# Kernel optimization log

Measured on AMD Instinct MI355X. Metric: run time of the kernel, lower is better.

Reference implementation:

```python
import jax, jax.numpy as jnp
import numpy as np

H = 1024      # hidden_dim
F = 4 * H     # expert FFN dim
E = 16        # num_experts
K = 4         # num_experts_per_token


def setup_inputs() -> dict:
    key = jax.random.key(0)
    ks = jax.random.split(key, 10)
    s = 0.02
    return {
        "x": jax.random.normal(ks[0], (2, 1024, H), dtype=jnp.float32),
        # router: Linear(H,H) -> ReLU -> Linear(H,E)
        "Wr1": jax.random.normal(ks[1], (H, H), dtype=jnp.float32) * s,
        "br1": jnp.zeros((H,), dtype=jnp.float32),
        "Wr2": jax.random.normal(ks[2], (H, E), dtype=jnp.float32) * s,
        "br2": jnp.zeros((E,), dtype=jnp.float32),
        # stacked experts: Linear(H,4H) -> GELU -> Linear(4H,H)
        "W1": jax.random.normal(ks[3], (E, H, F), dtype=jnp.float32) * s,
        "b1": jnp.zeros((E, F), dtype=jnp.float32),
        "W2": jax.random.normal(ks[4], (E, F, H), dtype=jnp.float32) * s,
        "b2": jnp.zeros((E, H), dtype=jnp.float32),
    }


def reference(x, Wr1, br1, Wr2, br2, W1, b1, W2, b2):
    B, S, Hd = x.shape
    xf = x.reshape(-1, Hd)                       # [T, H]
    T = xf.shape[0]
    # router logits
    logits = jnp.maximum(xf @ Wr1 + br1, 0.0) @ Wr2 + br2   # [T, E]
    # top-k routing: softmax over the k selected logits
    topw, topi = jax.lax.top_k(logits, K)                    # [T, K]
    topw = jax.nn.softmax(topw, axis=-1)
    # dense combine weights c[t, e] = sum_k topw[t,k] * 1[topi[t,k]==e]
    c = jnp.zeros((T, E), dtype=xf.dtype)
    c = c.at[jnp.arange(T)[:, None], topi].add(topw)         # [T, E]
    # all-experts dense MLP (exact GELU, matching nn.GELU default)
    h = jax.nn.gelu(jnp.einsum('th,ehf->etf', xf, W1) + b1[:, None, :],
                    approximate=False)                       # [E, T, F]
    y = jnp.einsum('etf,efh->eth', h, W2) + b2[:, None, :]   # [E, T, H]
    out = jnp.einsum('eth,te->th', y, c)                     # [T, H]
    return out.reshape(B, S, Hd)
```

## Files before the change

### kernel.cpp

```cpp
#include <hip/hip_runtime.h>
#include <hip/hip_bf16.h>

#define T_TOK 2048
#define H_DIM 1024
#define F_DIM 4096
#define E_NUM 16
#define K_TOP 4

typedef float    floatx4 __attribute__((ext_vector_type(4)));
typedef _Float16 f16x8   __attribute__((ext_vector_type(8)));
typedef __fp16   fp16v2  __attribute__((ext_vector_type(2)));

#define MiB (1024ull * 1024ull)
#define LOGIT_OFF ((size_t)0)
#define OFFS_OFF  (256ull * 1024)
#define TOKS_OFF  (320ull * 1024)
#define WSL_OFF   (384ull * 1024)
#define STK_OFF   (448ull * 1024)
#define TILEE_OFF (512ull * 1024)
#define TILEM_OFF (TILEE_OFF + 512)
#define TILEC_OFF (TILEM_OFF + 512)
#define XH_OFF    (1ull * MiB)
#define HBUF_OFF  (8ull * MiB)
#define YBUF_OFF  (72ull * MiB)
#define WS_NEED_FAST (96ull * MiB)

__device__ __forceinline__ void gload16(const void* g, void* l) {
  __builtin_amdgcn_global_load_lds(
      (const __attribute__((address_space(1))) unsigned int*)g,
      (__attribute__((address_space(3))) unsigned int*)l, 16, 0, 0);
}

__device__ __forceinline__ float gelu_fast(float v) {
  float z = 0.7978845608028654f * (v + 0.044715f * v * v * v);
  float e = __expf(2.f * z);
  float t = 1.f - 2.f / (e + 1.f);
  return 0.5f * v * (1.f + t);
}

__device__ __forceinline__ void cast_x_body(int blk, const float* __restrict__ x,
                                            _Float16* __restrict__ xh) {
  int i = blk * 256 + threadIdx.x;
  const floatx4* xin = reinterpret_cast<const floatx4*>(x) + (size_t)i * 2;
  floatx4 a = xin[0], b = xin[1];
  f16x8 o;
  o[0] = (_Float16)a[0]; o[1] = (_Float16)a[1]; o[2] = (_Float16)a[2]; o[3] = (_Float16)a[3];
  o[4] = (_Float16)b[0]; o[5] = (_Float16)b[1]; o[6] = (_Float16)b[2]; o[7] = (_Float16)b[3];
  *reinterpret_cast<f16x8*>(xh + (size_t)i * 8) = o;
}

__device__ __forceinline__ void router_gemm1_body(
    int m0, int n0, const float* __restrict__ x, const float* __restrict__ Wr1,
    const float* __restrict__ br1, float* __restrict__ hrf, char* smem) {
  _Float16 (*Ah)[40] = (_Float16(*)[40])(smem);
  _Float16 (*Al)[40] = (_Float16(*)[40])(smem + 5120);
  _Float16 (*Bh)[40] = (_Float16(*)[40])(smem + 10240);
  _Float16 (*Bl)[40] = (_Float16(*)[40])(smem + 15360);
  int tid = threadIdx.x;
  int arow = tid >> 2, achk = tid & 3;
  const float* Arow = x + (size_t)(m0 + arow) * H_DIM + achk * 8;
  int brow = tid >> 3, bq = tid & 7;

  floatx4 acc[2][2];
#pragma unroll
  for (int i = 0; i < 2; i++)
#pragma unroll
    for (int j = 0; j < 2; j++) acc[i][j] = (floatx4){0.f, 0.f, 0.f, 0.f};

  int wv = tid >> 6, lane = tid & 63;
  int wm = wv >> 1, wn = wv & 1;
  int lrow = lane & 15, lk = (lane >> 4) * 8;

  for (int k0 = 0; k0 < H_DIM; k0 += 32) {
    floatx4 a0 = *reinterpret_cast<const floatx4*>(Arow + k0);
    floatx4 a1 = *reinterpret_cast<const floatx4*>(Arow + k0 + 4);
    f16x8 hv, lv;
#pragma unroll
    for (int j = 0; j < 4; j++) {
      _Float16 hi = (_Float16)a0[j]; hv[j] = hi; lv[j] = (_Float16)(a0[j] - (float)hi);
      _Float16 hi2 = (_Float16)a1[j]; hv[4 + j] = hi2; lv[4 + j] = (_Float16)(a1[j] - (float)hi2);
    }
    *reinterpret_cast<f16x8*>(&Ah[arow][achk * 8]) = hv;
    *reinterpret_cast<f16x8*>(&Al[arow][achk * 8]) = lv;
    const float* wp = Wr1 + (size_t)(k0 + brow) * H_DIM + n0 + bq * 4;
    floatx4 w0 = *reinterpret_cast<const floatx4*>(wp);
    floatx4 w1 = *reinterpret_cast<const floatx4*>(wp + 32);
#pragma unroll
    for (int i = 0; i < 4; i++) {
      _Float16 h0 = (_Float16)w0[i];
      Bh[bq * 4 + i][brow] = h0; Bl[bq * 4 + i][brow] = (_Float16)(w0[i] - (float)h0);
      _Float16 h1 = (_Float16)w1[i];
      Bh[32 + bq * 4 + i][brow] = h1; Bl[32 + bq * 4 + i][brow] = (_Float16)(w1[i] - (float)h1);
    }
    __syncthreads();

    f16x8 ah0 = *reinterpret_cast<const f16x8*>(&Ah[32 * wm + lrow][lk]);
    f16x8 ah1 = *reinterpret_cast<const f16x8*>(&Ah[32 * wm + 16 + lrow][lk]);
    f16x8 al0 = *reinterpret_cast<const f16x8*>(&Al[32 * wm + lrow][lk]);
    f16x8 al1 = *reinterpret_cast<const f16x8*>(&Al[32 * wm + 16 + lrow][lk]);
    f16x8 bh0 = *reinterpret_cast<const f16x8*>(&Bh[32 * wn + lrow][lk]);
    f16x8 bh1 = *reinterpret_cast<const f16x8*>(&Bh[32 * wn + 16 + lrow][lk]);
    f16x8 bl0 = *reinterpret_cast<const f16x8*>(&Bl[32 * wn + lrow][lk]);
    f16x8 bl1 = *reinterpret_cast<const f16x8*>(&Bl[32 * wn + 16 + lrow][lk]);

    acc[0][0] = __builtin_amdgcn_mfma_f32_16x16x32_f16(ah0, bh0, acc[0][0], 0, 0, 0);
    acc[0][0] = __builtin_amdgcn_mfma_f32_16x16x32_f16(ah0, bl0, acc[0][0], 0, 0, 0);
    acc[0][0] = __builtin_amdgcn_mfma_f32_16x16x32_f16(al0, bh0, acc[0][0], 0, 0, 0);
    acc[0][1] = __builtin_amdgcn_mfma_f32_16x16x32_f16(ah0, bh1, acc[0][1], 0, 0, 0);
    acc[0][1] = __builtin_amdgcn_mfma_f32_16x16x32_f16(ah0, bl1, acc[0][1], 0, 0, 0);
    acc[0][1] = __builtin_amdgcn_mfma_f32_16x16x32_f16(al0, bh1, acc[0][1], 0, 0, 0);
    acc[1][0] = __builtin_amdgcn_mfma_f32_16x16x32_f16(ah1, bh0, acc[1][0], 0, 0, 0);
    acc[1][0] = __builtin_amdgcn_mfma_f32_16x16x32_f16(ah1, bl0, acc[1][0], 0, 0, 0);
    acc[1][0] = __builtin_amdgcn_mfma_f32_16x16x32_f16(al1, bh0, acc[1][0], 0, 0, 0);
    acc[1][1] = __builtin_amdgcn_mfma_f32_16x16x32_f16(ah1, bh1, acc[1][1], 0, 0, 0);
    acc[1][1] = __builtin_amdgcn_mfma_f32_16x16x32_f16(ah1, bl1, acc[1][1], 0, 0, 0);
    acc[1][1] = __builtin_amdgcn_mfma_f32_16x16x32_f16(al1, bh1, acc[1][1], 0, 0, 0);
    __syncthreads();
  }

#pragma unroll
  for (int am = 0; am < 2; am++) {
#pragma unroll
    for (int bn = 0; bn < 2; bn++) {
      int col = n0 + 32 * wn + 16 * bn + lrow;
      float bv = br1[col];
#pragma unroll
      for (int r = 0; r < 4; r++) {
        int rowt = 32 * wm + 16 * am + (lane >> 4) * 4 + r;
        float v = acc[am][bn][r] + bv;
        hrf[(size_t)(m0 + rowt) * H_DIM + col] = fmaxf(v, 0.f);
      }
    }
  }
}

#define P1_RG 512
#define P1_CX 1024
#define P1_TOTAL (P1_RG + P1_CX)
__global__ __launch_bounds__(256) void fusedA_kernel(
    const float* __restrict__ x, const float* __restrict__ Wr1, const float* __restrict__ br1,
    float* __restrict__ hrf, _Float16* __restrict__ xh) {
  __shared__ __align__(16) char smem[20480];
  int bid = blockIdx.x;
  if (bid < P1_RG) {
    router_gemm1_body((bid >> 4) * 64, (bid & 15) * 64, x, Wr1, br1, hrf, smem);
  } else {
    cast_x_body(bid - P1_RG, x, xh);
  }
}

__global__ __launch_bounds__(256) void router_logits_kernel(
    const float* __restrict__ hrf, const float* __restrict__ Wr2,
    const float* __restrict__ br2, float* __restrict__ logits) {
  int t = blockIdx.x * 4 + (threadIdx.x >> 6);
  int lane = threadIdx.x & 63;
  float acc[E_NUM];
#pragma unroll
  for (int e = 0; e < E_NUM; e++) acc[e] = 0.f;
  const float* hr = hrf + (size_t)t * H_DIM;
#pragma unroll 4
  for (int i = 0; i < H_DIM / 64; i++) {
    int k = lane + 64 * i;
    float a = hr[k];
    const floatx4* w4 = reinterpret_cast<const floatx4*>(Wr2 + (size_t)k * E_NUM);
    floatx4 w0 = w4[0], w1 = w4[1], w2 = w4[2], w3 = w4[3];
#pragma unroll
    for (int j = 0; j < 4; j++) {
      acc[j]      += a * w0[j];
      acc[4 + j]  += a * w1[j];
      acc[8 + j]  += a * w2[j];
      acc[12 + j] += a * w3[j];
    }
  }
#pragma unroll
  for (int e = 0; e < E_NUM; e++) {
    float v = acc[e];
    for (int off = 32; off > 0; off >>= 1) v += __shfl_xor(v, off);
    if (lane == e) logits[(size_t)t * E_NUM + e] = v + br2[e];
  }
}

__global__ __launch_bounds__(1024) void routing_kernel(
    const float* __restrict__ logits, int* __restrict__ offs,
    int* __restrict__ toks, float* __restrict__ wsl, int* __restrict__ stk,
    int* __restrict__ tileE, int* __restrict__ tileM, int* __restrict__ tileC) {
  __shared__ int cnt[E_NUM], cur[E_NUM], loff[E_NUM + 1];
  int tid = threadIdx.x;
  if (tid < E_NUM) { cnt[tid] = 0; cur[tid] = 0; }
  __syncthreads();
  int ti[2][K_TOP]; float tw[2][K_TOP];
#pragma unroll
  for (int u = 0; u < 2; u++) {
    int t = u * 1024 + tid;
    float lg[E_NUM];
#pragma unroll
    for (int e = 0; e < E_NUM; e++) lg[e] = logits[(size_t)t * E_NUM + e];
    unsigned int used = 0;
    float vals[K_TOP];
#pragma unroll
    for (int k = 0; k < K_TOP; k++) {
      float best = -1e30f; int bi = 0;
#pragma unroll
      for (int e = 0; e < E_NUM; e++) {
        if (!((used >> e) & 1u) && lg[e] > best) { best = lg[e]; bi = e; }
      }
      used |= (1u << bi);
      vals[k] = best; ti[u][k] = bi;
    }
    float m = vals[0], s = 0.f;
#pragma unroll
    for (int k = 0; k < K_TOP; k++) { tw[u][k] = expf(vals[k] - m); s += tw[u][k]; }
    float inv = 1.f / s;
#pragma unroll
    for (int k = 0; k < K_TOP; k++) {
      tw[u][k] *= inv;
      atomicAdd(&cnt[ti[u][k]], 1);
    }
  }
  __syncthreads();
  if (tid == 0) {
    int acc = 0;
    loff[0] = 0; offs[0] = 0;
    for (int e = 0; e < E_NUM; e++) { acc += cnt[e]; loff[e + 1] = acc; offs[e + 1] = acc; }
    int idx = 0;
    for (int e = 0; e < E_NUM; e++) {
      for (int m0 = 0; m0 < cnt[e]; m0 += 128) { tileE[idx] = e; tileM[idx] = m0; idx++; }
    }
    tileC[0] = idx;
  }
  __syncthreads();
#pragma unroll
  for (int u = 0; u < 2; u++) {
    int t = u * 1024 + tid;
#pragma unroll
    for (int k = 0; k < K_TOP; k++) {
      int e = ti[u][k];
      int pos = atomicAdd(&cur[e], 1);
      int slot = loff[e] + pos;
      toks[slot] = t;
      wsl[slot] = tw[u][k];
      stk[t * K_TOP + k] = slot;
    }
  }
}

__global__ void combine_kernel(const _Float16* __restrict__ ybuf, const int* __restrict__ stk,
                               float* __restrict__ out) {
  int i = blockIdx.x * 256 + threadIdx.x;
  size_t p = (size_t)i * 8;
  int t = (int)(p >> 10);
  int h = (int)(p & 1023);
  float s[8] = {0.f, 0.f, 0.f, 0.f, 0.f, 0.f, 0.f, 0.f};
#pragma unroll
  for (int k = 0; k < K_TOP; k++) {
    int slot = stk[t * K_TOP + k];
    f16x8 v = *reinterpret_cast<const f16x8*>(ybuf + (size_t)slot * H_DIM + h);
#pragma unroll
    for (int j = 0; j < 8; j++) s[j] += (float)v[j];
  }
  floatx4 o0 = {s[0], s[1], s[2], s[3]};
  floatx4 o1 = {s[4], s[5], s[6], s[7]};
  *reinterpret_cast<floatx4*>(out + p) = o0;
  *reinterpret_cast<floatx4*>(out + p + 4) = o1;
}

template <int KK, int ACT, bool GATHER, bool SCALE>
__device__ __forceinline__ void moe_gemm_body(
    int ti, int n0, const _Float16* __restrict__ A, const float* __restrict__ Bf,
    const float* __restrict__ bias, _Float16* __restrict__ Out,
    const int* __restrict__ offsets, const int* __restrict__ toklist,
    const float* __restrict__ wslot, const int* __restrict__ tileE,
    const int* __restrict__ tileM, const int* __restrict__ tileC,
    int N, char* smem) {
  if (ti >= tileC[0]) return;
  const int K = KK;
  int e = tileE[ti], m0 = tileM[ti];
  int base = offsets[e], cnt = offsets[e + 1] - base;

  _Float16 (*As)[128][32] = reinterpret_cast<_Float16(*)[128][32]>(smem);
  float (*Bs)[32][128] = reinterpret_cast<float(*)[32][128]>(smem + 24576);

  int tid = threadIdx.x;
  int w = tid >> 6, lane = tid & 63;
  int wm = w >> 1, wn = w & 1;
  int lrow = lane & 15, hi = lane >> 4;

  int ar0 = w * 32 + (lane >> 2);
  int ar1 = ar0 + 16;
  int ach = (((lane & 3) ^ ((lane >> 3) & 3))) * 8;
  int mr0 = m0 + ar0; if (mr0 >= cnt) mr0 = cnt - 1;
  int mr1 = m0 + ar1; if (mr1 >= cnt) mr1 = cnt - 1;
  const _Float16* gA0 = A + (long)(GATHER ? toklist[base + mr0] : (base + mr0)) * K + ach;
  const _Float16* gA1 = A + (long)(GATHER ? toklist[base + mr1] : (base + mr1)) * K + ach;
  const float* Bfe = Bf + (size_t)e * (size_t)K * (size_t)N;
  const float* gB = Bfe + (size_t)(8 * w + (lane >> 5)) * N + n0 +
                    ((((lane & 31) ^ ((w & 1) << 2))) << 2);

  int phys8 = ((lane >> 4) ^ ((lrow >> 1) & 3)) * 8;
  int bswz = (hi & 1) << 4;

#define STAGE3(buf, kk) do { \
    gload16(gA0 + (kk), &As[buf][w * 32][0]); \
    gload16(gA1 + (kk), &As[buf][w * 32 + 16][0]); \
    gload16(gB + (size_t)(kk) * N,         &Bs[buf][8 * w + 0][0]); \
    gload16(gB + (size_t)(kk) * N + 2 * N, &Bs[buf][8 * w + 2][0]); \
    gload16(gB + (size_t)(kk) * N + 4 * N, &Bs[buf][8 * w + 4][0]); \
    gload16(gB + (size_t)(kk) * N + 6 * N, &Bs[buf][8 * w + 6][0]); \
  } while (0)

#define COMPUTE3(buf) do { \
    f16x8 a[4], b[4]; \
    _Pragma("unroll") \
    for (int i = 0; i < 4; i++) \
      a[i] = *reinterpret_cast<const f16x8*>(&As[buf][wm * 64 + i * 16 + lrow][phys8]); \
    _Pragma("unroll") \
    for (int i = 0; i < 4; i++) { \
      int pcol = (wn * 64 + i * 16 + lrow) ^ bswz; \
      float f0 = Bs[buf][hi * 8 + 0][pcol]; \
      float f1 = Bs[buf][hi * 8 + 1][pcol]; \
      float f2 = Bs[buf][hi * 8 + 2][pcol]; \
      float f3 = Bs[buf][hi * 8 + 3][pcol]; \
      float f4 = Bs[buf][hi * 8 + 4][pcol]; \
      float f5 = Bs[buf][hi * 8 + 5][pcol]; \
      float f6 = Bs[buf][hi * 8 + 6][pcol]; \
      float f7 = Bs[buf][hi * 8 + 7][pcol]; \
      union { fp16v2 h[4]; f16x8 v; } u; \
      u.h[0] = __builtin_amdgcn_cvt_pkrtz(f0, f1); \
      u.h[1] = __builtin_amdgcn_cvt_pkrtz(f2, f3); \
      u.h[2] = __builtin_amdgcn_cvt_pkrtz(f4, f5); \
      u.h[3] = __builtin_amdgcn_cvt_pkrtz(f6, f7); \
      b[i] = u.v; \
    } \
    __builtin_amdgcn_s_setprio(1); \
    _Pragma("unroll") \
    for (int i = 0; i < 4; i++) \
      _Pragma("unroll") \
      for (int j = 0; j < 4; j++) \
        acc[i][j] = __builtin_amdgcn_mfma_f32_16x16x32_f16(a[i], b[j], acc[i][j], 0, 0, 0); \
    __builtin_amdgcn_s_setprio(0); \
  } while (0)

  floatx4 acc[4][4];
#pragma unroll
  for (int i = 0; i < 4; i++)
#pragma unroll
    for (int j = 0; j < 4; j++) acc[i][j] = (floatx4){0.f, 0.f, 0.f, 0.f};

  constexpr int nk = KK / 32;
  STAGE3(0, 0);
  STAGE3(1, 32);

#pragma unroll 3
  for (int it = 0; it < nk - 1; ++it) {
    asm volatile("s_waitcnt vmcnt(6)" ::: "memory");
    __builtin_amdgcn_s_barrier();
    if (it + 2 < nk) STAGE3((it + 2) % 3, (it + 2) * 32);
    COMPUTE3(it % 3);
  }
  asm volatile("s_waitcnt vmcnt(0)" ::: "memory");
  __builtin_amdgcn_s_barrier();
  COMPUTE3((nk - 1) % 3);

#undef STAGE3
#undef COMPUTE3

  const float* be = bias + (size_t)e * N;
#pragma unroll
  for (int fm = 0; fm < 4; fm++) {
#pragma unroll
    for (int fn = 0; fn < 4; fn++) {
      int col = n0 + wn * 64 + fn * 16 + lrow;
      float bv = be[col];
#pragma unroll
      for (int r = 0; r < 4; r++) {
        int rowt = wm * 64 + fm * 16 + (lane >> 4) * 4 + r;
        int mg = m0 + rowt;
        if (mg < cnt) {
          float v = acc[fm][fn][r] + bv;
          if (ACT == 2) v = gelu_fast(v);
          long orow = base + mg;
          if (SCALE) v *= wslot[orow];
          Out[orow * (long)N + col] = (_Float16)v;
        }
      }
    }
  }
}

__global__ __launch_bounds__(256) void moe_gemm1_kernel(
    const _Float16* __restrict__ xh, const float* __restrict__ W1,
    const float* __restrict__ b1, _Float16* __restrict__ hbuf,
    const int* __restrict__ offsets, const int* __restrict__ toklist,
    const int* __restrict__ tileE, const int* __restrict__ tileM, const int* __restrict__ tileC) {
  __shared__ __align__(16) char smem[73728];
  int x = blockIdx.x;
  int ti = (x & 7) * 10 + (x >> 3);
  moe_gemm_body<H_DIM, 2, true, false>(ti, blockIdx.y * 128, xh, W1, b1, hbuf,
                                       offsets, toklist, nullptr, tileE, tileM, tileC,
                                       F_DIM, smem);
}

__global__ __launch_bounds__(256) void moe_gemm2_kernel(
    const _Float16* __restrict__ hbuf, const float* __restrict__ W2,
    const float* __restrict__ b2, _Float16* __restrict__ ybuf,
    const int* __restrict__ offsets, const float* __restrict__ wslot,
    const int* __restrict__ tileE, const int* __restrict__ tileM, const int* __restrict__ tileC) {
  __shared__ __align__(16) char smem[73728];
  int x = blockIdx.x;
  int ti = (x & 7) * 10 + (x >> 3);
  moe_gemm_body<F_DIM, 0, false, true>(ti, blockIdx.y * 128, hbuf, W2, b2, ybuf,
                                       offsets, nullptr, wslot, tileE, tileM, tileC,
                                       H_DIM, smem);
}

template <int ACT, bool GATHER, bool OFFS, bool SCALE>
__global__ __launch_bounds__(256) void moe_gemm(
    const _Float16* __restrict__ A, const float* __restrict__ W,
    const float* __restrict__ bias, _Float16* __restrict__ Out,
    const int* __restrict__ offsets, const int* __restrict__ toklist,
    const float* __restrict__ wslot, int M, int N, int K) {
  int e = blockIdx.z;
  int base = 0, cnt = M;
  if (OFFS) { base = offsets[e]; cnt = offsets[e + 1] - base; }
  int m0 = blockIdx.y * 64;
  if (m0 >= cnt) return;
  int n0 = blockIdx.x * 64;
  const float* We = W + (size_t)e * K * N;
  const float* be = bias + (size_t)e * N;

  __shared__ _Float16 As[64][40];
  __shared__ _Float16 Bs[64][40];

  int tid = threadIdx.x;
  int arow = tid >> 2, achk = tid & 3;
  int am_idx = m0 + arow; if (am_idx > cnt - 1) am_idx = cnt - 1;
  long arowg = GATHER ? (long)toklist[base + am_idx] : (long)(base + am_idx);
  const _Float16* Arow = A + arowg * (long)K + achk * 8;

  int brow = tid >> 3, bq = tid & 7;

  floatx4 acc[2][2];
#pragma unroll
  for (int i = 0; i < 2; i++)
#pragma unroll
    for (int j = 0; j < 2; j++) acc[i][j] = (floatx4){0.f, 0.f, 0.f, 0.f};

  int wv = tid >> 6, lane = tid & 63;
  int wm = wv >> 1, wn = wv & 1;
  int lrow = lane & 15, lk = (lane >> 4) * 8;

  for (int k0 = 0; k0 < K; k0 += 32) {
    *reinterpret_cast<f16x8*>(&As[arow][achk * 8]) = *reinterpret_cast<const f16x8*>(Arow + k0);
    const float* wp = We + (size_t)(k0 + brow) * N + n0 + bq * 4;
    floatx4 w0 = *reinterpret_cast<const floatx4*>(wp);
    floatx4 w1 = *reinterpret_cast<const floatx4*>(wp + 32);
#pragma unroll
    for (int i = 0; i < 4; i++) {
      Bs[bq * 4 + i][brow]      = (_Float16)w0[i];
      Bs[32 + bq * 4 + i][brow] = (_Float16)w1[i];
    }
    __syncthreads();

    f16x8 a0 = *reinterpret_cast<const f16x8*>(&As[32 * wm + lrow][lk]);
    f16x8 a1 = *reinterpret_cast<const f16x8*>(&As[32 * wm + 16 + lrow][lk]);
    f16x8 b0 = *reinterpret_cast<const f16x8*>(&Bs[32 * wn + lrow][lk]);
    f16x8 b1 = *reinterpret_cast<const f16x8*>(&Bs[32 * wn + 16 + lrow][lk]);
    acc[0][0] = __builtin_amdgcn_mfma_f32_16x16x32_f16(a0, b0, acc[0][0], 0, 0, 0);
    acc[0][1] = __builtin_amdgcn_mfma_f32_16x16x32_f16(a0, b1, acc[0][1], 0, 0, 0);
    acc[1][0] = __builtin_amdgcn_mfma_f32_16x16x32_f16(a1, b0, acc[1][0], 0, 0, 0);
    acc[1][1] = __builtin_amdgcn_mfma_f32_16x16x32_f16(a1, b1, acc[1][1], 0, 0, 0);
    __syncthreads();
  }

#pragma unroll
  for (int am = 0; am < 2; am++) {
#pragma unroll
    for (int bn = 0; bn < 2; bn++) {
      int col = n0 + 32 * wn + 16 * bn + lrow;
      float bv = be[col];
#pragma unroll
      for (int r = 0; r < 4; r++) {
        int rowt = 32 * wm + 16 * am + (lane >> 4) * 4 + r;
        int mg = m0 + rowt;
        if (mg < cnt) {
          float v = acc[am][bn][r] + bv;
          if (ACT == 2) v = gelu_fast(v);
          long orow = base + mg;
          if (SCALE) v *= wslot[orow];
          Out[orow * (long)N + col] = (_Float16)v;
        }
      }
    }
  }
}

__global__ void cast_x_kernel(const float* __restrict__ x, _Float16* __restrict__ xh) {
  cast_x_body(blockIdx.x, x, xh);
}

__global__ __launch_bounds__(256) void router_gemm1_kernel(
    const float* __restrict__ x, const float* __restrict__ Wr1,
    const float* __restrict__ br1, float* __restrict__ hrf) {
  __shared__ __align__(16) char smem[20480];
  router_gemm1_body(blockIdx.y * 64, blockIdx.x * 64, x, Wr1, br1, hrf, smem);
}

extern "C" void kernel_launch(void* const* d_in, const int* in_sizes, int n_in,
                              void* d_out, int out_size, void* d_ws, size_t ws_size,
                              hipStream_t stream) {
  const float* x   = (const float*)d_in[0];
  const float* Wr1 = (const float*)d_in[1];
  const float* br1 = (const float*)d_in[2];
  const float* Wr2 = (const float*)d_in[3];
  const float* br2 = (const float*)d_in[4];
  const float* W1  = (const float*)d_in[5];
  const float* b1  = (const float*)d_in[6];
  const float* W2  = (const float*)d_in[7];
  const float* b2  = (const float*)d_in[8];
  float* out = (float*)d_out;

  char* ws = (char*)d_ws;
  float* logits = (float*)(ws + LOGIT_OFF);
  int*   offs   = (int*)(ws + OFFS_OFF);
  int*   toks   = (int*)(ws + TOKS_OFF);
  float* wsl    = (float*)(ws + WSL_OFF);
  int*   stk    = (int*)(ws + STK_OFF);
  int*   tileE  = (int*)(ws + TILEE_OFF);
  int*   tileM  = (int*)(ws + TILEM_OFF);
  int*   tileC  = (int*)(ws + TILEC_OFF);
  _Float16* xh   = (_Float16*)(ws + XH_OFF);
  float*    hrf  = (float*)(ws + HBUF_OFF);
  _Float16* hbuf = (_Float16*)(ws + HBUF_OFF);
  _Float16* ybuf = (_Float16*)(ws + YBUF_OFF);

  bool fast = ws_size >= WS_NEED_FAST;

  if (fast) {
    fusedA_kernel<<<P1_TOTAL, 256, 0, stream>>>(x, Wr1, br1, hrf, xh);
  } else {
    cast_x_kernel<<<(T_TOK * H_DIM / 8) / 256, 256, 0, stream>>>(x, xh);
    router_gemm1_kernel<<<dim3(H_DIM / 64, T_TOK / 64), 256, 0, stream>>>(x, Wr1, br1, hrf);
  }

  router_logits_kernel<<<T_TOK / 4, 256, 0, stream>>>(hrf, Wr2, br2, logits);
  routing_kernel<<<1, 1024, 0, stream>>>(logits, offs, toks, wsl, stk, tileE, tileM, tileC);

  if (fast) {
    moe_gemm1_kernel<<<dim3(80, F_DIM / 128), 256, 0, stream>>>(xh, W1, b1, hbuf, offs, toks,
                                                                tileE, tileM, tileC);
    moe_gemm2_kernel<<<dim3(80, H_DIM / 128), 256, 0, stream>>>(hbuf, W2, b2, ybuf, offs, wsl,
                                                                tileE, tileM, tileC);
  } else {
    moe_gemm<2, true, true, false><<<dim3(F_DIM / 64, T_TOK / 64, E_NUM), 256, 0, stream>>>(
        xh, W1, b1, hbuf, offs, toks, nullptr, T_TOK, F_DIM, H_DIM);
    moe_gemm<0, false, true, true><<<dim3(H_DIM / 64, T_TOK / 64, E_NUM), 256, 0, stream>>>(
        hbuf, W2, b2, ybuf, offs, nullptr, wsl, T_TOK, H_DIM, F_DIM);
  }

  combine_kernel<<<(T_TOK * H_DIM / 8) / 256, 256, 0, stream>>>(ybuf, stk, out);
}
```

Measured before the change: 485.9 us.

## Convert B tiles to fp16 in registers before LDS, use double buffering

Weight tiles are now loaded from global memory into registers, converted to fp16 once, and written to LDS in a padded k-packed layout. The MFMA B operand is then a single vector LDS read instead of eight scalar fp32 reads plus conversions per fragment. The three-stage async pipeline becomes a two-stage register-staged double buffer with full vmcnt/lgkmcnt waits, which cuts LDS use and may raise occupancy but exposes more load latency. The swizzled tile-index block mapping is also dropped in favour of plain blockIdx.x.

```diff
diff --git a/kernel.cpp b/kernel.cpp
--- a/kernel.cpp
+++ b/kernel.cpp
@@ -278,7 +278,7 @@
   int base = offsets[e], cnt = offsets[e + 1] - base;
 
   _Float16 (*As)[128][32] = reinterpret_cast<_Float16(*)[128][32]>(smem);
-  float (*Bs)[32][128] = reinterpret_cast<float(*)[32][128]>(smem + 24576);
+  _Float16 (*Bs)[4][130][8] = reinterpret_cast<_Float16(*)[4][130][8]>(smem + 16384);
 
   int tid = threadIdx.x;
   int w = tid >> 6, lane = tid & 63;
@@ -292,44 +292,43 @@
   int mr1 = m0 + ar1; if (mr1 >= cnt) mr1 = cnt - 1;
   const _Float16* gA0 = A + (long)(GATHER ? toklist[base + mr0] : (base + mr0)) * K + ach;
   const _Float16* gA1 = A + (long)(GATHER ? toklist[base + mr1] : (base + mr1)) * K + ach;
+  int phys8 = ((lane >> 4) ^ ((lrow >> 1) & 3)) * 8;
+
   const float* Bfe = Bf + (size_t)e * (size_t)K * (size_t)N;
-  const float* gB = Bfe + (size_t)(8 * w + (lane >> 5)) * N + n0 +
-                    ((((lane & 31) ^ ((w & 1) << 2))) << 2);
-
-  int phys8 = ((lane >> 4) ^ ((lrow >> 1) & 3)) * 8;
-  int bswz = (hi & 1) << 4;
-
-#define STAGE3(buf, kk) do { \
+  const float* gBb = Bfe + (size_t)(8 * w) * N + n0 + lane;
+
+  float br0[16], br1[16];
+
+#define BLOAD(kk, br) do { \
+    _Pragma("unroll") \
+    for (int h = 0; h < 2; h++) \
+      _Pragma("unroll") \
+      for (int j = 0; j < 8; j++) \
+        br[h * 8 + j] = gBb[(size_t)((kk) + j) * N + 64 * h]; \
+  } while (0)
+
+#define BWRITE(buf, br) do { \
+    _Pragma("unroll") \
+    for (int h = 0; h < 2; h++) { \
+      union { fp16v2 h2[4]; f16x8 v; } u; \
+      _Pragma("unroll") \
+      for (int p = 0; p < 4; p++) \
+        u.h2[p] = __builtin_amdgcn_cvt_pkrtz(br[h * 8 + 2 * p], br[h * 8 + 2 * p + 1]); \
+      *reinterpret_cast<f16x8*>(&Bs[buf][w][lane + 64 * h][0]) = u.v; \
+    } \
+  } while (0)
+
+#define STAGEA(buf, kk) do { \
     gload16(gA0 + (kk), &As[buf][w * 32][0]); \
     gload16(gA1 + (kk), &As[buf][w * 32 + 16][0]); \
-    gload16(gB + (size_t)(kk) * N,         &Bs[buf][8 * w + 0][0]); \
-    gload16(gB + (size_t)(kk) * N + 2 * N, &Bs[buf][8 * w + 2][0]); \
-    gload16(gB + (size_t)(kk) * N + 4 * N, &Bs[buf][8 * w + 4][0]); \
-    gload16(gB + (size_t)(kk) * N + 6 * N, &Bs[buf][8 * w + 6][0]); \
   } while (0)
 
-#define COMPUTE3(buf) do { \
+#define COMPUTE(buf) do { \
     f16x8 a[4], b[4]; \
     _Pragma("unroll") \
-    for (int i = 0; i < 4; i++) \
+    for (int i = 0; i < 4; i++) { \
       a[i] = *reinterpret_cast<const f16x8*>(&As[buf][wm * 64 + i * 16 + lrow][phys8]); \
-    _Pragma("unroll") \
-    for (int i = 0; i < 4; i++) { \
-      int pcol = (wn * 64 + i * 16 + lrow) ^ bswz; \
-      float f0 = Bs[buf][hi * 8 + 0][pcol]; \
-      float f1 = Bs[buf][hi * 8 + 1][pcol]; \
-      float f2 = Bs[buf][hi * 8 + 2][pcol]; \
-      float f3 = Bs[buf][hi * 8 + 3][pcol]; \
-      float f4 = Bs[buf][hi * 8 + 4][pcol]; \
-      float f5 = Bs[buf][hi * 8 + 5][pcol]; \
-      float f6 = Bs[buf][hi * 8 + 6][pcol]; \
-      float f7 = Bs[buf][hi * 8 + 7][pcol]; \
-      union { fp16v2 h[4]; f16x8 v; } u; \
-      u.h[0] = __builtin_amdgcn_cvt_pkrtz(f0, f1); \
-      u.h[1] = __builtin_amdgcn_cvt_pkrtz(f2, f3); \
-      u.h[2] = __builtin_amdgcn_cvt_pkrtz(f4, f5); \
-      u.h[3] = __builtin_amdgcn_cvt_pkrtz(f6, f7); \
-      b[i] = u.v; \
+      b[i] = *reinterpret_cast<const f16x8*>(&Bs[buf][hi][wn * 64 + i * 16 + lrow][0]); \
     } \
     __builtin_amdgcn_s_setprio(1); \
     _Pragma("unroll") \
@@ -347,22 +346,28 @@
     for (int j = 0; j < 4; j++) acc[i][j] = (floatx4){0.f, 0.f, 0.f, 0.f};
 
   constexpr int nk = KK / 32;
-  STAGE3(0, 0);
-  STAGE3(1, 32);
-
-#pragma unroll 3
-  for (int it = 0; it < nk - 1; ++it) {
-    asm volatile("s_waitcnt vmcnt(6)" ::: "memory");
+  BLOAD(0, br0);
+  STAGEA(0, 0);
+
+  for (int it = 0; it < nk; it += 2) {
+    BWRITE(0, br0);
+    asm volatile("s_waitcnt vmcnt(0)" ::: "memory");
+    asm volatile("s_waitcnt lgkmcnt(0)" ::: "memory");
     __builtin_amdgcn_s_barrier();
-    if (it + 2 < nk) STAGE3((it + 2) % 3, (it + 2) * 32);
-    COMPUTE3(it % 3);
-  }
-  asm volatile("s_waitcnt vmcnt(0)" ::: "memory");
-  __builtin_amdgcn_s_barrier();
-  COMPUTE3((nk - 1) % 3);
-
-#undef STAGE3
-#undef COMPUTE3
+    if (it + 1 < nk) { BLOAD((it + 1) * 32, br1); STAGEA(1, (it + 1) * 32); }
+    COMPUTE(0);
+    BWRITE(1, br1);
+    asm volatile("s_waitcnt vmcnt(0)" ::: "memory");
+    asm volatile("s_waitcnt lgkmcnt(0)" ::: "memory");
+    __builtin_amdgcn_s_barrier();
+    if (it + 2 < nk) { BLOAD((it + 2) * 32, br0); STAGEA(0, (it + 2) * 32); }
+    COMPUTE(1);
+  }
+
+#undef BLOAD
+#undef BWRITE
+#undef STAGEA
+#undef COMPUTE
 
   const float* be = bias + (size_t)e * N;
 #pragma unroll
@@ -392,10 +397,8 @@
     const float* __restrict__ b1, _Float16* __restrict__ hbuf,
     const int* __restrict__ offsets, const int* __restrict__ toklist,
     const int* __restrict__ tileE, const int* __restrict__ tileM, const int* __restrict__ tileC) {
-  __shared__ __align__(16) char smem[73728];
-  int x = blockIdx.x;
-  int ti = (x & 7) * 10 + (x >> 3);
-  moe_gemm_body<H_DIM, 2, true, false>(ti, blockIdx.y * 128, xh, W1, b1, hbuf,
+  __shared__ __align__(16) char smem[33280];
+  moe_gemm_body<H_DIM, 2, true, false>(blockIdx.x, blockIdx.y * 128, xh, W1, b1, hbuf,
                                        offsets, toklist, nullptr, tileE, tileM, tileC,
                                        F_DIM, smem);
 }
@@ -405,10 +408,8 @@
     const float* __restrict__ b2, _Float16* __restrict__ ybuf,
     const int* __restrict__ offsets, const float* __restrict__ wslot,
     const int* __restrict__ tileE, const int* __restrict__ tileM, const int* __restrict__ tileC) {
-  __shared__ __align__(16) char smem[73728];
-  int x = blockIdx.x;
-  int ti = (x & 7) * 10 + (x >> 3);
-  moe_gemm_body<F_DIM, 0, false, true>(ti, blockIdx.y * 128, hbuf, W2, b2, ybuf,
+  __shared__ __align__(16) char smem[33280];
+  moe_gemm_body<F_DIM, 0, false, true>(blockIdx.x, blockIdx.y * 128, hbuf, W2, b2, ybuf,
                                        offsets, nullptr, wslot, tileE, tileM, tileC,
                                        H_DIM, smem);
 }
```

After: 582.7 us. 1.2x slower.
